# Performance work log

Hardware: AMD Instinct MI355X
Metric: run time of the kernel (lower is better)

The kernel has to match this reference:

```python
import jax, jax.numpy as jnp
import numpy as np

N_NODES = 100000
N_EDGES = 1000000
D = 128


def setup_inputs() -> dict:
    key = jax.random.key(0)
    k1, k2, k3, k4 = jax.random.split(key, 4)
    x = jax.random.normal(k1, (N_NODES, D), dtype=jnp.float32)
    src = jax.random.randint(k2, (N_EDGES,), 0, N_NODES, dtype=jnp.int64)
    dst = jax.random.randint(k3, (N_EDGES,), 0, N_NODES, dtype=jnp.int64)
    # nn.Linear(2*D, 1): weight [1, 2*D], bias [1]
    W = jax.random.normal(k4, (1, 2 * D), dtype=jnp.float32) / np.sqrt(2 * D)
    b = jnp.zeros((1,), dtype=jnp.float32)
    return {"x": x, "src": src, "dst": dst, "W": W, "b": b}


def reference(x, src, dst, W, b):
    # cat([x[src], x[dst]], 1) @ W.T + b  ==  x[src] @ w_s + x[dst] @ w_d + b
    w_s = W[0, :D]   # [D]
    w_d = W[0, D:]   # [D]
    logits = x[src] @ w_s + x[dst] @ w_d + b[0]  # [E]
    return jax.nn.sigmoid(logits)  # squeezed score per edge
```

## Files before the change

### kernel.cpp

```cpp
#include <hip/hip_runtime.h>
#include <math.h>


#define DIM 128

__global__ __launch_bounds__(256) void proj_kernel(
    const float* __restrict__ x,
    const float* __restrict__ W,
    float* __restrict__ ps,
    float* __restrict__ pd,
    int n_nodes)
{
    const int half = threadIdx.x >> 5;
    const int lane = threadIdx.x & 31;
    const int node = blockIdx.x * 8 + half;
    if (node >= n_nodes) return;

    const float4* x4 = (const float4*)x + (size_t)node * (DIM / 4) + lane;
    float4 v = *x4;

    const float4* w4 = (const float4*)W;
    float4 ws = w4[lane];
    float4 wd = w4[32 + lane];

    float s = v.x * ws.x + v.y * ws.y + v.z * ws.z + v.w * ws.w;
    float d = v.x * wd.x + v.y * wd.y + v.z * wd.z + v.w * wd.w;

    #pragma unroll
    for (int off = 16; off > 0; off >>= 1) {
        s += __shfl_down(s, off, 32);
        d += __shfl_down(d, off, 32);
    }
    if (lane == 0) {
        ps[node] = s;
        pd[node] = d;
    }
}

__global__ __launch_bounds__(256) void edge_kernel(
    const int* __restrict__ src,
    const int* __restrict__ dst,
    const float* __restrict__ ps,
    const float* __restrict__ pd,
    const float* __restrict__ b,
    float* __restrict__ out,
    int n_edges)
{
    const int e = blockIdx.x * blockDim.x + threadIdx.x;
    if (e >= n_edges) return;
    const float z = ps[src[e]] + pd[dst[e]] + b[0];
    out[e] = 1.0f / (1.0f + __expf(-z));
}

extern "C" void kernel_launch(void* const* d_in, const int* in_sizes, int n_in,
                              void* d_out, int out_size, void* d_ws, size_t ws_size,
                              hipStream_t stream) {
    const float* x   = (const float*)d_in[0];
    const int*   src = (const int*)d_in[1];
    const int*   dst = (const int*)d_in[2];
    const float* W   = (const float*)d_in[3];
    const float* b   = (const float*)d_in[4];
    float* out = (float*)d_out;

    const int n_nodes = in_sizes[0] / DIM;
    const int n_edges = in_sizes[1];

    float* ps = (float*)d_ws;
    float* pd = ps + n_nodes;

    proj_kernel<<<(n_nodes + 7) / 8, 256, 0, stream>>>(x, W, ps, pd, n_nodes);
    edge_kernel<<<(n_edges + 255) / 256, 256, 0, stream>>>(src, dst, ps, pd, b, out, n_edges);
}
```

Baseline: 103.0 us.

## Use grid-stride 8-lane node projection and vectorized 4-edge processing

The projection kernel now gives each node to 8 lanes that each load four float4 values, keeps the weights in registers, and grid-strides over nodes with a capped block count. This replaces the 32-lane shuffle reduction with a shorter 8-lane one. The edge kernel now handles four edges per thread using int4 index loads and float4 stores, with one thread handling the tail. The intent is to raise memory-level parallelism and cut per-edge instruction overhead. The trade-off is fewer total threads for the gathers.

```diff
diff --git a/kernel.cpp b/kernel.cpp
--- a/kernel.cpp
+++ b/kernel.cpp
@@ -11,29 +11,43 @@
     float* __restrict__ pd,
     int n_nodes)
 {
-    const int half = threadIdx.x >> 5;
-    const int lane = threadIdx.x & 31;
-    const int node = blockIdx.x * 8 + half;
-    if (node >= n_nodes) return;
+    const int j = threadIdx.x & 7;
+    const int G = (blockIdx.x * blockDim.x + threadIdx.x) >> 3;
+    const int stride = (gridDim.x * blockDim.x) >> 3;
 
-    const float4* x4 = (const float4*)x + (size_t)node * (DIM / 4) + lane;
-    float4 v = *x4;
+    const float4* __restrict__ x4 = (const float4*)x;
+    const float4* __restrict__ w4 = (const float4*)W;
 
-    const float4* w4 = (const float4*)W;
-    float4 ws = w4[lane];
-    float4 wd = w4[32 + lane];
+    const float4 ws0 = w4[j],      ws1 = w4[8 + j],
+                 ws2 = w4[16 + j], ws3 = w4[24 + j];
+    const float4 wd0 = w4[32 + j],      wd1 = w4[40 + j],
+                 wd2 = w4[48 + j],      wd3 = w4[56 + j];
 
-    float s = v.x * ws.x + v.y * ws.y + v.z * ws.z + v.w * ws.w;
-    float d = v.x * wd.x + v.y * wd.y + v.z * wd.z + v.w * wd.w;
+    for (int node = G; node < n_nodes; node += stride) {
+        const size_t base = (size_t)node * (DIM / 4);
+        float4 v0 = x4[base + 0 * 8 + j];
+        float4 v1 = x4[base + 1 * 8 + j];
+        float4 v2 = x4[base + 2 * 8 + j];
+        float4 v3 = x4[base + 3 * 8 + j];
 
-    #pragma unroll
-    for (int off = 16; off > 0; off >>= 1) {
-        s += __shfl_down(s, off, 32);
-        d += __shfl_down(d, off, 32);
-    }
-    if (lane == 0) {
-        ps[node] = s;
-        pd[node] = d;
+        float s = v0.x * ws0.x + v0.y * ws0.y + v0.z * ws0.z + v0.w * ws0.w
+                + v1.x * ws1.x + v1.y * ws1.y + v1.z * ws1.z + v1.w * ws1.w
+                + v2.x * ws2.x + v2.y * ws2.y + v2.z * ws2.z + v2.w * ws2.w
+                + v3.x * ws3.x + v3.y * ws3.y + v3.z * ws3.z + v3.w * ws3.w;
+        float d = v0.x * wd0.x + v0.y * wd0.y + v0.z * wd0.z + v0.w * wd0.w
+                + v1.x * wd1.x + v1.y * wd1.y + v1.z * wd1.z + v1.w * wd1.w
+                + v2.x * wd2.x + v2.y * wd2.y + v2.z * wd2.z + v2.w * wd2.w
+                + v3.x * wd3.x + v3.y * wd3.y + v3.z * wd3.z + v3.w * wd3.w;
+
+        #pragma unroll
+        for (int off = 4; off > 0; off >>= 1) {
+            s += __shfl_down(s, off, 8);
+            d += __shfl_down(d, off, 8);
+        }
+        if (j == 0) {
+            ps[node] = s;
+            pd[node] = d;
+        }
     }
 }
 
@@ -46,10 +60,29 @@
     float* __restrict__ out,
     int n_edges)
 {
-    const int e = blockIdx.x * blockDim.x + threadIdx.x;
-    if (e >= n_edges) return;
-    const float z = ps[src[e]] + pd[dst[e]] + b[0];
-    out[e] = 1.0f / (1.0f + __expf(-z));
+    const int nQuad = n_edges >> 2;
+    const int q = blockIdx.x * blockDim.x + threadIdx.x;
+    const float bb = b[0];
+
+    if (q < nQuad) {
+        const int4 s4 = ((const int4*)src)[q];
+        const int4 d4 = ((const int4*)dst)[q];
+        const float z0 = ps[s4.x] + pd[d4.x] + bb;
+        const float z1 = ps[s4.y] + pd[d4.y] + bb;
+        const float z2 = ps[s4.z] + pd[d4.z] + bb;
+        const float z3 = ps[s4.w] + pd[d4.w] + bb;
+        float4 o;
+        o.x = 1.0f / (1.0f + __expf(-z0));
+        o.y = 1.0f / (1.0f + __expf(-z1));
+        o.z = 1.0f / (1.0f + __expf(-z2));
+        o.w = 1.0f / (1.0f + __expf(-z3));
+        ((float4*)out)[q] = o;
+    } else if (q == nQuad) {
+        for (int e = nQuad * 4; e < n_edges; ++e) {
+            const float z = ps[src[e]] + pd[dst[e]] + bb;
+            out[e] = 1.0f / (1.0f + __expf(-z));
+        }
+    }
 }
 
 extern "C" void kernel_launch(void* const* d_in, const int* in_sizes, int n_in,
@@ -68,6 +101,11 @@
     float* ps = (float*)d_ws;
     float* pd = ps + n_nodes;
 
-    proj_kernel<<<(n_nodes + 7) / 8, 256, 0, stream>>>(x, W, ps, pd, n_nodes);
-    edge_kernel<<<(n_edges + 255) / 256, 256, 0, stream>>>(src, dst, ps, pd, b, out, n_edges);
+    int proj_blocks = (n_nodes + 31) / 32;
+    if (proj_blocks > 1024) proj_blocks = 1024;
+    proj_kernel<<<proj_blocks, 256, 0, stream>>>(x, W, ps, pd, n_nodes);
+
+    const int nQuad = n_edges >> 2;
+    const int edge_blocks = (nQuad + 1 + 255) / 256;
+    edge_kernel<<<edge_blocks, 256, 0, stream>>>(src, dst, ps, pd, b, out, n_edges);
 }
```

Result: no change. 102.6 us (-0.4%).
